# Optimization experiments

Measured on AMD Instinct MI355X. Metric: run time of the kernel, lower is better.

## Reference

```python
import jax, jax.numpy as jnp
import numpy as np

B, N, NUM = 16384, 512, 3  # batch, num queries, num vanishing points per image


def setup_inputs() -> dict:
    key = jax.random.key(0)
    k1, k2, k3 = jax.random.split(key, 3)
    pred_logits = jax.random.normal(k1, (B, N, 1), jnp.float32)
    pp = jax.random.normal(k2, (B, N, 3), jnp.float32)
    pred_pos = pp / jnp.linalg.norm(pp, axis=-1, keepdims=True)  # unit directions
    vp = jax.random.normal(k3, (B, 3, NUM), jnp.float32)
    vps_unique = vp / jnp.linalg.norm(vp, axis=1, keepdims=True)  # all columns valid (abs-sum > 1e-5)
    return {"pred_logits": pred_logits, "pred_pos": pred_pos, "vps_unique": vps_unique}


def _greedy_select(conf, pos, num):
    # conf: [N,1], pos: [N,3]; greedy angular NMS keeping `num` candidates.
    order = jnp.argsort(-conf[:, 0]).astype(jnp.int32)  # descending confidence
    thresh = jnp.pi / (num + 1)
    ar = jnp.arange(num)
    cand0 = jnp.zeros((num,), jnp.int32).at[0].set(order[0])

    def step(carry, idx):
        cand, count = carry
        sel = pos[cand]                                   # [num,3]
        dots = jnp.minimum(jnp.abs(sel @ pos[idx]), 1.0)  # clip for arccos stability
        ang = jnp.where(ar < count, jnp.arccos(dots), jnp.inf)
        add = (count < num) & (jnp.min(ang) >= thresh)    # torch: skip if dst < pi/(num+1)
        cand = jnp.where(add & (ar == count), idx, cand)
        return (cand, count + add.astype(jnp.int32)), None

    (cand, _), _ = jax.lax.scan(step, (cand0, jnp.int32(1)), order[1:])
    return pos[cand]  # [num,3]


def reference(pred_logits, pred_pos, vps_unique):
    num = vps_unique.shape[2]  # static: all vps columns are valid by construction
    sel = jax.vmap(lambda c, p: _greedy_select(c, p, num))(pred_logits, pred_pos)
    return sel  # [B, num, 3]
```

## Files before the change

### kernel.cpp

```cpp
#include <hip/hip_runtime.h>
#include <math.h>

#define B_TOTAL 16384
#define NQ 512
#define NUM 3

__global__ __launch_bounds__(256, 8) void greedy_nms_kernel(
    const float* __restrict__ conf,
    const float* __restrict__ pos,
    float* __restrict__ out)
{
    const int lane = threadIdx.x & 63;
    const int b = (blockIdx.x << 2) | (threadIdx.x >> 6);

    const float* cb = conf + (size_t)b * NQ;
    const float* pb = pos  + (size_t)b * NQ * 3;

    const float4* cb4 = reinterpret_cast<const float4*>(cb);
    float4 c0 = cb4[lane * 2 + 0];
    float4 c1 = cb4[lane * 2 + 1];
    const float4* pb4 = reinterpret_cast<const float4*>(pb);
    float4 q0 = pb4[lane * 6 + 0];
    float4 q1 = pb4[lane * 6 + 1];
    float4 q2 = pb4[lane * 6 + 2];
    float4 q3 = pb4[lane * 6 + 3];
    float4 q4 = pb4[lane * 6 + 4];
    float4 q5 = pb4[lane * 6 + 5];

    unsigned k[8];
    {
        float f[8] = {c0.x, c0.y, c0.z, c0.w, c1.x, c1.y, c1.z, c1.w};
        #pragma unroll
        for (int s = 0; s < 8; ++s) {
            int bi = __float_as_int(f[s]);
            k[s] = (unsigned)bi ^ ((unsigned)(bi >> 31) | 0x80000000u);
        }
    }

    float rx[8], ry[8], rz[8];
    rx[0] = q0.x; ry[0] = q0.y; rz[0] = q0.z;
    rx[1] = q0.w; ry[1] = q1.x; rz[1] = q1.y;
    rx[2] = q1.z; ry[2] = q1.w; rz[2] = q2.x;
    rx[3] = q2.y; ry[3] = q2.z; rz[3] = q2.w;
    rx[4] = q3.x; ry[4] = q3.y; rz[4] = q3.z;
    rx[5] = q3.w; ry[5] = q4.x; rz[5] = q4.y;
    rx[6] = q4.z; ry[6] = q4.w; rz[6] = q5.x;
    rx[7] = q5.y; ry[7] = q5.z; rz[7] = q5.w;

    auto argmax64 = [&]() -> unsigned long long {
        bool s01 = k[1] > k[0];
        unsigned m01 = s01 ? k[1] : k[0]; int i01 = s01 ? 1 : 0;
        bool s23 = k[3] > k[2];
        unsigned m23 = s23 ? k[3] : k[2]; int i23 = s23 ? 3 : 2;
        bool s45 = k[5] > k[4];
        unsigned m45 = s45 ? k[5] : k[4]; int i45 = s45 ? 5 : 4;
        bool s67 = k[7] > k[6];
        unsigned m67 = s67 ? k[7] : k[6]; int i67 = s67 ? 7 : 6;
        if (m23 > m01) { m01 = m23; i01 = i23; }
        if (m67 > m45) { m45 = m67; i45 = i67; }
        if (m45 > m01) { m01 = m45; i01 = i45; }
        unsigned long long key =
            ((unsigned long long)m01 << 32) |
            (unsigned)(NQ - 1 - ((lane << 3) + i01));
        #pragma unroll
        for (int off = 1; off < 64; off <<= 1) {
            unsigned long long o = __shfl_xor(key, off);
            if (o > key) key = o;
        }
        return key;
    };

    auto get_row = [&](int w, float& x, float& y, float& z) {
        const int ow = w >> 3, sl = w & 7;
        float tx = rx[0], ty = ry[0], tz = rz[0];
        #pragma unroll
        for (int s = 1; s < 8; ++s)
            if (sl == s) { tx = rx[s]; ty = ry[s]; tz = rz[s]; }
        x = __shfl(tx, ow); y = __shfl(ty, ow); z = __shfl(tz, ow);
    };

    const float TH  = 0.78539816339744830961f;
    const float CLO = 0.70710478f;
    const float CHI = 0.70710878f;

    auto mask_keys = [&](float px, float py, float pz) {
        #pragma unroll
        for (int s = 0; s < 8; ++s) {
            float d = fabsf(rx[s] * px + ry[s] * py + rz[s] * pz);
            bool pass;
            if (d <= CLO)      pass = true;
            else if (d >= CHI) pass = false;
            else               pass = (acosf(fminf(d, 1.f)) >= TH);
            if (!pass) k[s] = 0u;
        }
    };

    unsigned long long K1 = argmax64();
    const int w1 = NQ - 1 - (int)(K1 & 0x1ffu);
    float p1x, p1y, p1z;
    get_row(w1, p1x, p1y, p1z);
    {
        const int osl = ((w1 >> 3) == lane) ? (w1 & 7) : 8;
        #pragma unroll
        for (int s = 0; s < 8; ++s)
            if (osl == s) k[s] = 0u;
    }

    mask_keys(p1x, p1y, p1z);
    unsigned long long K2 = argmax64();

    float o2x, o2y, o2z, o3x, o3y, o3z;
    if ((unsigned)(K2 >> 32) != 0u) {
        const int w2 = NQ - 1 - (int)(K2 & 0x1ffu);
        get_row(w2, o2x, o2y, o2z);
        mask_keys(o2x, o2y, o2z);
        unsigned long long K3 = argmax64();
        if ((unsigned)(K3 >> 32) != 0u) {
            const int w3 = NQ - 1 - (int)(K3 & 0x1ffu);
            get_row(w3, o3x, o3y, o3z);
        } else {
            get_row(0, o3x, o3y, o3z);
        }
    } else {
        get_row(0, o2x, o2y, o2z);
        o3x = o2x; o3y = o2y; o3z = o2z;
    }

    if (lane == 0) {
        float* ob = out + (size_t)b * 9;
        ob[0] = p1x; ob[1] = p1y; ob[2] = p1z;
        ob[3] = o2x; ob[4] = o2y; ob[5] = o2z;
        ob[6] = o3x; ob[7] = o3y; ob[8] = o3z;
    }
}

extern "C" void kernel_launch(void* const* d_in, const int* in_sizes, int n_in,
                              void* d_out, int out_size, void* d_ws, size_t ws_size,
                              hipStream_t stream) {
    const float* pred_logits = (const float*)d_in[0];
    const float* pred_pos    = (const float*)d_in[1];
    float* out = (float*)d_out;

    const int grid = B_TOTAL / 4;
    greedy_nms_kernel<<<grid, 256, 0, stream>>>(pred_logits, pred_pos, out);
}
```

Before: 32.88 us.

## Stage positions in LDS and stride element ownership across lanes

Positions are now loaded coalesced (float4 per lane at stride 64) and written to a per-wave LDS buffer, and confidences are loaded as strided scalars so each lane owns elements i*64+lane. Row lookup becomes a direct LDS read instead of a register select plus shuffle, and masking reads positions from LDS. This removes the per-lane 96-byte contiguous loads and the register-heavy shuffle path. In exchange it adds 24KB of LDS per block, a __syncthreads, and LDS reads with stride-3 bank patterns in the mask loop. The occupancy hint in the launch bounds is also dropped, and the LDS footprint may limit how many blocks fit per CU.

```diff
diff --git a/kernel.cpp b/kernel.cpp
--- a/kernel.cpp
+++ b/kernel.cpp
@@ -5,63 +5,57 @@
 #define NQ 512
 #define NUM 3
 
-__global__ __launch_bounds__(256, 8) void greedy_nms_kernel(
+__global__ __launch_bounds__(256) void greedy_nms_kernel(
     const float* __restrict__ conf,
     const float* __restrict__ pos,
     float* __restrict__ out)
 {
+    __shared__ float lds[4 * NQ * 3];
     const int lane = threadIdx.x & 63;
-    const int b = (blockIdx.x << 2) | (threadIdx.x >> 6);
+    const int wv   = threadIdx.x >> 6;
+    const int b    = (blockIdx.x << 2) | wv;
 
     const float* cb = conf + (size_t)b * NQ;
     const float* pb = pos  + (size_t)b * NQ * 3;
+    float* wl = lds + wv * (NQ * 3);
 
-    const float4* cb4 = reinterpret_cast<const float4*>(cb);
-    float4 c0 = cb4[lane * 2 + 0];
-    float4 c1 = cb4[lane * 2 + 1];
     const float4* pb4 = reinterpret_cast<const float4*>(pb);
-    float4 q0 = pb4[lane * 6 + 0];
-    float4 q1 = pb4[lane * 6 + 1];
-    float4 q2 = pb4[lane * 6 + 2];
-    float4 q3 = pb4[lane * 6 + 3];
-    float4 q4 = pb4[lane * 6 + 4];
-    float4 q5 = pb4[lane * 6 + 5];
+    float4 t0 = pb4[0 * 64 + lane];
+    float4 t1 = pb4[1 * 64 + lane];
+    float4 t2 = pb4[2 * 64 + lane];
+    float4 t3 = pb4[3 * 64 + lane];
+    float4 t4 = pb4[4 * 64 + lane];
+    float4 t5 = pb4[5 * 64 + lane];
+
+    float c[8];
+    #pragma unroll
+    for (int i = 0; i < 8; ++i) c[i] = cb[i * 64 + lane];
+
+    float4* wl4 = reinterpret_cast<float4*>(wl);
+    wl4[0 * 64 + lane] = t0;
+    wl4[1 * 64 + lane] = t1;
+    wl4[2 * 64 + lane] = t2;
+    wl4[3 * 64 + lane] = t3;
+    wl4[4 * 64 + lane] = t4;
+    wl4[5 * 64 + lane] = t5;
 
     unsigned k[8];
-    {
-        float f[8] = {c0.x, c0.y, c0.z, c0.w, c1.x, c1.y, c1.z, c1.w};
-        #pragma unroll
-        for (int s = 0; s < 8; ++s) {
-            int bi = __float_as_int(f[s]);
-            k[s] = (unsigned)bi ^ ((unsigned)(bi >> 31) | 0x80000000u);
-        }
+    #pragma unroll
+    for (int i = 0; i < 8; ++i) {
+        int bi = __float_as_int(c[i]);
+        k[i] = (unsigned)bi ^ ((unsigned)(bi >> 31) | 0x80000000u);
     }
 
-    float rx[8], ry[8], rz[8];
-    rx[0] = q0.x; ry[0] = q0.y; rz[0] = q0.z;
-    rx[1] = q0.w; ry[1] = q1.x; rz[1] = q1.y;
-    rx[2] = q1.z; ry[2] = q1.w; rz[2] = q2.x;
-    rx[3] = q2.y; ry[3] = q2.z; rz[3] = q2.w;
-    rx[4] = q3.x; ry[4] = q3.y; rz[4] = q3.z;
-    rx[5] = q3.w; ry[5] = q4.x; rz[5] = q4.y;
-    rx[6] = q4.z; ry[6] = q4.w; rz[6] = q5.x;
-    rx[7] = q5.y; ry[7] = q5.z; rz[7] = q5.w;
+    __syncthreads();
 
     auto argmax64 = [&]() -> unsigned long long {
-        bool s01 = k[1] > k[0];
-        unsigned m01 = s01 ? k[1] : k[0]; int i01 = s01 ? 1 : 0;
-        bool s23 = k[3] > k[2];
-        unsigned m23 = s23 ? k[3] : k[2]; int i23 = s23 ? 3 : 2;
-        bool s45 = k[5] > k[4];
-        unsigned m45 = s45 ? k[5] : k[4]; int i45 = s45 ? 5 : 4;
-        bool s67 = k[7] > k[6];
-        unsigned m67 = s67 ? k[7] : k[6]; int i67 = s67 ? 7 : 6;
-        if (m23 > m01) { m01 = m23; i01 = i23; }
-        if (m67 > m45) { m45 = m67; i45 = i67; }
-        if (m45 > m01) { m01 = m45; i01 = i45; }
+        unsigned m = k[0]; int im = 0;
+        #pragma unroll
+        for (int i = 1; i < 8; ++i)
+            if (k[i] > m) { m = k[i]; im = i; }
         unsigned long long key =
-            ((unsigned long long)m01 << 32) |
-            (unsigned)(NQ - 1 - ((lane << 3) + i01));
+            ((unsigned long long)m << 32) |
+            (unsigned)(NQ - 1 - (im * 64 + lane));
         #pragma unroll
         for (int off = 1; off < 64; off <<= 1) {
             unsigned long long o = __shfl_xor(key, off);
@@ -70,13 +64,8 @@
         return key;
     };
 
-    auto get_row = [&](int w, float& x, float& y, float& z) {
-        const int ow = w >> 3, sl = w & 7;
-        float tx = rx[0], ty = ry[0], tz = rz[0];
-        #pragma unroll
-        for (int s = 1; s < 8; ++s)
-            if (sl == s) { tx = rx[s]; ty = ry[s]; tz = rz[s]; }
-        x = __shfl(tx, ow); y = __shfl(ty, ow); z = __shfl(tz, ow);
+    auto get_row = [&](int n, float& x, float& y, float& z) {
+        x = wl[3 * n + 0]; y = wl[3 * n + 1]; z = wl[3 * n + 2];
     };
 
     const float TH  = 0.78539816339744830961f;
@@ -85,13 +74,15 @@
 
     auto mask_keys = [&](float px, float py, float pz) {
         #pragma unroll
-        for (int s = 0; s < 8; ++s) {
-            float d = fabsf(rx[s] * px + ry[s] * py + rz[s] * pz);
+        for (int i = 0; i < 8; ++i) {
+            const int o = 3 * (i * 64 + lane);
+            float x = wl[o + 0], y = wl[o + 1], z = wl[o + 2];
+            float d = fabsf(x * px + y * py + z * pz);
             bool pass;
             if (d <= CLO)      pass = true;
             else if (d >= CHI) pass = false;
             else               pass = (acosf(fminf(d, 1.f)) >= TH);
-            if (!pass) k[s] = 0u;
+            if (!pass) k[i] = 0u;
         }
     };
 
@@ -100,10 +91,10 @@
     float p1x, p1y, p1z;
     get_row(w1, p1x, p1y, p1z);
     {
-        const int osl = ((w1 >> 3) == lane) ? (w1 & 7) : 8;
+        const int ci = ((w1 & 63) == lane) ? (w1 >> 6) : 8;
         #pragma unroll
-        for (int s = 0; s < 8; ++s)
-            if (osl == s) k[s] = 0u;
+        for (int i = 0; i < 8; ++i)
+            if (ci == i) k[i] = 0u;
     }
 
     mask_keys(p1x, p1y, p1z);
```

Result: faster. 26.94 us (-18.1%).

## Select top-8 by confidence first and gather only needed positions

Applied to the files above, without the earlier changes.

The kernel no longer loads all 512 position vectors per image. It runs eight wave-wide argmax passes over the confidence keys to get the top-8 candidates and gathers only their positions. The greedy angular NMS then runs over those eight with ballots, and a sequential fallback loop fetches further positions only if fewer than three survivors are found. This cuts position-array traffic, which dominated a memory-bound kernel, in exchange for extra shuffle reductions and scattered small gathers. The occupancy hint in launch bounds is also dropped.

```diff
diff --git a/kernel.cpp b/kernel.cpp
--- a/kernel.cpp
+++ b/kernel.cpp
@@ -4,8 +4,9 @@
 #define B_TOTAL 16384
 #define NQ 512
 #define NUM 3
+#define TOPK 8
 
-__global__ __launch_bounds__(256, 8) void greedy_nms_kernel(
+__global__ __launch_bounds__(256) void greedy_nms_kernel(
     const float* __restrict__ conf,
     const float* __restrict__ pos,
     float* __restrict__ out)
@@ -19,13 +20,7 @@
     const float4* cb4 = reinterpret_cast<const float4*>(cb);
     float4 c0 = cb4[lane * 2 + 0];
     float4 c1 = cb4[lane * 2 + 1];
-    const float4* pb4 = reinterpret_cast<const float4*>(pb);
-    float4 q0 = pb4[lane * 6 + 0];
-    float4 q1 = pb4[lane * 6 + 1];
-    float4 q2 = pb4[lane * 6 + 2];
-    float4 q3 = pb4[lane * 6 + 3];
-    float4 q4 = pb4[lane * 6 + 4];
-    float4 q5 = pb4[lane * 6 + 5];
+    const float p0x = pb[0], p0y = pb[1], p0z = pb[2];
 
     unsigned k[8];
     {
@@ -36,16 +31,6 @@
             k[s] = (unsigned)bi ^ ((unsigned)(bi >> 31) | 0x80000000u);
         }
     }
-
-    float rx[8], ry[8], rz[8];
-    rx[0] = q0.x; ry[0] = q0.y; rz[0] = q0.z;
-    rx[1] = q0.w; ry[1] = q1.x; rz[1] = q1.y;
-    rx[2] = q1.z; ry[2] = q1.w; rz[2] = q2.x;
-    rx[3] = q2.y; ry[3] = q2.z; rz[3] = q2.w;
-    rx[4] = q3.x; ry[4] = q3.y; rz[4] = q3.z;
-    rx[5] = q3.w; ry[5] = q4.x; rz[5] = q4.y;
-    rx[6] = q4.z; ry[6] = q4.w; rz[6] = q5.x;
-    rx[7] = q5.y; ry[7] = q5.z; rz[7] = q5.w;
 
     auto argmax64 = [&]() -> unsigned long long {
         bool s01 = k[1] > k[0];
@@ -70,60 +55,92 @@
         return key;
     };
 
-    auto get_row = [&](int w, float& x, float& y, float& z) {
-        const int ow = w >> 3, sl = w & 7;
-        float tx = rx[0], ty = ry[0], tz = rz[0];
+    auto consume = [&](int n) {
+        const int osl = ((n >> 3) == lane) ? (n & 7) : 8;
         #pragma unroll
-        for (int s = 1; s < 8; ++s)
-            if (sl == s) { tx = rx[s]; ty = ry[s]; tz = rz[s]; }
-        x = __shfl(tx, ow); y = __shfl(ty, ow); z = __shfl(tz, ow);
+        for (int s = 0; s < 8; ++s)
+            if (osl == s) k[s] = 0u;
     };
+
+    int myw = 0;
+    #pragma unroll
+    for (int i = 0; i < TOPK; ++i) {
+        unsigned long long K = argmax64();
+        const int n = NQ - 1 - (int)(K & 0x1ffu);
+        if (lane == i) myw = n;
+        consume(n);
+    }
+
+    float cx = pb[myw * 3 + 0];
+    float cy = pb[myw * 3 + 1];
+    float cz = pb[myw * 3 + 2];
 
     const float TH  = 0.78539816339744830961f;
     const float CLO = 0.70710478f;
     const float CHI = 0.70710878f;
 
-    auto mask_keys = [&](float px, float py, float pz) {
-        #pragma unroll
-        for (int s = 0; s < 8; ++s) {
-            float d = fabsf(rx[s] * px + ry[s] * py + rz[s] * pz);
-            bool pass;
-            if (d <= CLO)      pass = true;
-            else if (d >= CHI) pass = false;
-            else               pass = (acosf(fminf(d, 1.f)) >= TH);
-            if (!pass) k[s] = 0u;
-        }
+    auto pass1 = [&](float ax, float ay, float az,
+                     float px, float py, float pz) -> bool {
+        float d = fabsf(ax * px + ay * py + az * pz);
+        if (d <= CLO) return true;
+        if (d >= CHI) return false;
+        return acosf(fminf(d, 1.f)) >= TH;
     };
 
-    unsigned long long K1 = argmax64();
-    const int w1 = NQ - 1 - (int)(K1 & 0x1ffu);
-    float p1x, p1y, p1z;
-    get_row(w1, p1x, p1y, p1z);
-    {
-        const int osl = ((w1 >> 3) == lane) ? (w1 & 7) : 8;
-        #pragma unroll
-        for (int s = 0; s < 8; ++s)
-            if (osl == s) k[s] = 0u;
+    const float p1x = __shfl(cx, 0), p1y = __shfl(cy, 0), p1z = __shfl(cz, 0);
+    unsigned long long ball1 =
+        __ballot(pass1(p1x, p1y, p1z, cx, cy, cz)) & 0xFEull;
+
+    float o2x = p0x, o2y = p0y, o2z = p0z;
+    float o3x = p0x, o3y = p0y, o3z = p0z;
+    bool need_fallback;
+    float a1x = 0.f, a1y = 0.f, a1z = 0.f;
+    int count = 1;
+
+    if (ball1 != 0) {
+        const int i2 = __ffsll(ball1) - 1;
+        const float p2x = __shfl(cx, i2), p2y = __shfl(cy, i2),
+                    p2z = __shfl(cz, i2);
+        o2x = p2x; o2y = p2y; o2z = p2z;
+        a1x = p2x; a1y = p2y; a1z = p2z;
+        count = 2;
+        unsigned long long ball3 =
+            ball1 & __ballot(pass1(p2x, p2y, p2z, cx, cy, cz))
+                  & ~((2ull << i2) - 1);
+        if (ball3 != 0) {
+            const int i3 = __ffsll(ball3) - 1;
+            o3x = __shfl(cx, i3); o3y = __shfl(cy, i3); o3z = __shfl(cz, i3);
+            need_fallback = false;
+        } else {
+            need_fallback = true;
+        }
+    } else {
+        need_fallback = true;
     }
 
-    mask_keys(p1x, p1y, p1z);
-    unsigned long long K2 = argmax64();
-
-    float o2x, o2y, o2z, o3x, o3y, o3z;
-    if ((unsigned)(K2 >> 32) != 0u) {
-        const int w2 = NQ - 1 - (int)(K2 & 0x1ffu);
-        get_row(w2, o2x, o2y, o2z);
-        mask_keys(o2x, o2y, o2z);
-        unsigned long long K3 = argmax64();
-        if ((unsigned)(K3 >> 32) != 0u) {
-            const int w3 = NQ - 1 - (int)(K3 & 0x1ffu);
-            get_row(w3, o3x, o3y, o3z);
-        } else {
-            get_row(0, o3x, o3y, o3z);
+    if (need_fallback) {
+        #pragma unroll 1
+        for (int it = TOPK; it < NQ; ++it) {
+            unsigned long long K = argmax64();
+            if ((unsigned)(K >> 32) == 0u) break;
+            const int n = NQ - 1 - (int)(K & 0x1ffu);
+            consume(n);
+            const float px = pb[n * 3 + 0];
+            const float py = pb[n * 3 + 1];
+            const float pz = pb[n * 3 + 2];
+            bool add = pass1(p1x, p1y, p1z, px, py, pz) &&
+                       pass1(a1x, a1y, a1z, px, py, pz);
+            if (add) {
+                if (count == 1) {
+                    o2x = px; o2y = py; o2z = pz;
+                    a1x = px; a1y = py; a1z = pz;
+                    count = 2;
+                } else {
+                    o3x = px; o3y = py; o3z = pz;
+                    break;
+                }
+            }
         }
-    } else {
-        get_row(0, o2x, o2y, o2z);
-        o3x = o2x; o3y = o2y; o3z = o2z;
     }
 
     if (lane == 0) {
```

Result: no change. 32.52 us (-1.1%).
